# Kernel optimization log

Measured on AMD Instinct MI355X. Metric: run time of the kernel, lower is better.

Reference implementation:

```python
import jax, jax.numpy as jnp
import numpy as np
from math import sqrt

RATIOS = [0.5, 1.0, 2.0]
SCALES = [128.0, 256.0, 512.0]
STRIDE = 16
NA = 9  # len(RATIOS) * len(SCALES)


def _anchor_template():
    # matches RPNHead.__init__: center at stride/2, w = s/sqrt(r), h = s*sqrt(r)
    t = np.zeros((NA, 4), np.float32)
    for ri, r in enumerate(RATIOS):
        for si, s in enumerate(SCALES):
            i = ri * len(RATIOS) + si
            sr = sqrt(r)
            t[i] = [STRIDE / 2.0, STRIDE / 2.0, s / sr, s * sr]
    return jnp.asarray(t)


def _conv(x, w, b, pad):
    y = jax.lax.conv_general_dilated(
        x, w, window_strides=(1, 1), padding=[(pad, pad), (pad, pad)],
        dimension_numbers=('NCHW', 'OIHW', 'NCHW'))
    return y + b[None, :, None, None]


def setup_inputs() -> dict:
    key = jax.random.key(0)
    ks = jax.random.split(key, 5)
    B, C, H, W = 8, 512, 64, 64
    return {
        'feature_maps': jax.random.normal(ks[0], (B, C, H, W), jnp.float32),
        'img_size': jnp.ones((B, 2), jnp.int32) * 1024,  # (width, height) per image
        'conv_w': jax.random.normal(ks[1], (512, 512, 3, 3), jnp.float32) * 0.01,
        'conv_b': jnp.zeros((512,), jnp.float32),
        'cls_w': jax.random.normal(ks[2], (2 * NA, 512, 1, 1), jnp.float32) * 0.01,
        'cls_b': jnp.zeros((2 * NA,), jnp.float32),
        'reg_w': jax.random.normal(ks[3], (4 * NA, 512, 1, 1), jnp.float32) * 0.01,
        'reg_b': jnp.zeros((4 * NA,), jnp.float32),
    }


def reference(feature_maps, img_size, conv_w, conv_b, cls_w, cls_b, reg_w, reg_b):
    f = jax.nn.relu(_conv(feature_maps, conv_w, conv_b, 1))  # [B,512,H,W]
    B, _, H, W = f.shape
    # heads, NCHW -> NHWC, split anchor dim
    cls = _conv(f, cls_w, cls_b, 0).transpose(0, 2, 3, 1).reshape(B, H, W, NA, 2)
    reg = _conv(f, reg_w, reg_b, 0).transpose(0, 2, 3, 1).reshape(B, H, W, NA, 4)

    # generate_anchors (eval mode: anchors_ignore stays zero)
    tmpl = _anchor_template()  # [NA,4] xywh
    gy, gx = jnp.meshgrid(jnp.arange(H), jnp.arange(W), indexing='ij')
    center = jnp.stack([gx, gy], axis=-1).astype(jnp.float32) * STRIDE  # [H,W,2] (x,y)
    axy = tmpl[None, None, :, :2] + center[:, :, None, :]               # [H,W,NA,2]
    awh = jnp.broadcast_to(tmpl[None, None, :, 2:], (H, W, NA, 2))
    anchors = jnp.concatenate([axy, awh], axis=-1).reshape(-1, 4)       # [A,4]

    A = anchors.shape[0]
    reg = reg.reshape(B, A, 4)
    cls_scores = cls.reshape(B, A, 2)

    # anchor2bbox: inverse of the delta encoding in loss()
    ax, ay, aw, ah = anchors[:, 0], anchors[:, 1], anchors[:, 2], anchors[:, 3]
    px = ax[None, :] + reg[..., 0] * aw[None, :]
    py = ay[None, :] + reg[..., 1] * ah[None, :]
    pw = aw[None, :] * jnp.exp(reg[..., 2])
    ph = ah[None, :] * jnp.exp(reg[..., 3])
    imw = img_size[:, 0:1].astype(jnp.float32)
    imh = img_size[:, 1:2].astype(jnp.float32)
    x1 = jnp.clip(px - pw / 2, 0.0, imw)
    y1 = jnp.clip(py - ph / 2, 0.0, imh)
    x2 = jnp.clip(px + pw / 2, 0.0, imw)
    y2 = jnp.clip(py + ph / 2, 0.0, imh)
    proposals = jnp.stack([x1, y1, x2, y2], axis=-1)  # [B,A,4]

    anchors_ignore = jnp.zeros((B, A), jnp.int32)
    return (proposals, cls_scores, anchors_ignore)
```

## Files before the change

kernel.cpp:

```cpp
#include <hip/hip_runtime.h>
#include <hip/hip_bf16.h>
#include <stdint.h>

typedef __attribute__((ext_vector_type(4))) float f32x4;
typedef __attribute__((ext_vector_type(8))) short short8;

#define NB 8
#define NC 512
#define HP 66
#define WP 66
#define NPOS 32768
#define KTOT 4608
#define NKT 72

#define XP_ELEMS (NB*HP*WP*NC)
#define WR_ELEMS (NC*KTOT)
#define WC2_ELEMS (64*NC)
#define PROP_OFF 0
#define CLS_OFF  1179648
#define A_PER_B  36864

__device__ __forceinline__ short bf16bits(float v) {
    __hip_bfloat16 b = __float2bfloat16(v);
    return *reinterpret_cast<short*>(&b);
}
__device__ __forceinline__ void gload16(const short* g, short* l) {
    __builtin_amdgcn_global_load_lds(
        (const __attribute__((address_space(1))) unsigned int*)g,
        (__attribute__((address_space(3))) unsigned int*)l, 16, 0, 0);
}
#define BARRIER() asm volatile("s_barrier" ::: "memory")
#define VMCNT4()  asm volatile("s_waitcnt vmcnt(4)" ::: "memory")
#define VMCNT0()  asm volatile("s_waitcnt vmcnt(0)" ::: "memory")

__global__ void prep_input(const float* __restrict__ x, short* __restrict__ Xp) {
    __shared__ float t[64][65];
    const int pb = blockIdx.x, cb = blockIdx.y, b = blockIdx.z;
    const int tid = threadIdx.x;
    const int tx = tid & 63, ty = tid >> 6;
    const float* src = x + ((size_t)(b*NC + cb*64))*4096 + pb*64;
#pragma unroll
    for (int r = 0; r < 16; ++r) {
        int ch = ty + r*4;
        t[ch][tx] = src[(size_t)ch*4096 + tx];
    }
    __syncthreads();
#pragma unroll
    for (int rr = 0; rr < 2; ++rr) {
        int item = tid + rr*256;
        int pl = item >> 3, ck = item & 7;
        short8 v;
#pragma unroll
        for (int e = 0; e < 8; ++e) v[e] = bf16bits(t[ck*8+e][pl]);
        *(short8*)&Xp[((size_t)((b*HP + pb + 1)*WP) + (pl + 1))*NC + cb*64 + ck*8] = v;
    }
}

__global__ void prep_w(const float* __restrict__ w, short* __restrict__ Wr) {
    __shared__ float t[4608];
    const int o = blockIdx.x;
    const int tid = threadIdx.x;
    const float* src = w + (size_t)o*4608;
    for (int i = tid; i < 4608; i += 256) t[i] = src[i];
    __syncthreads();
#pragma unroll
    for (int k = 0; k < 9; ++k) {
#pragma unroll
        for (int c = 0; c < 2; ++c) {
            int ci = tid + c*256;
            Wr[(size_t)o*4608 + k*512 + ci] = bf16bits(t[ci*9 + k]);
        }
    }
}

__global__ void prep_w2(const float* __restrict__ cls_w, const float* __restrict__ reg_w,
                        short* __restrict__ Wc2) {
    int tid = blockIdx.x*256 + threadIdx.x;
    int row = tid >> 9, ci = tid & 511;
    float v = 0.f;
    if (row < 18)      v = cls_w[row*NC + ci];
    else if (row < 54) v = reg_w[(row-18)*NC + ci];
    Wc2[tid] = bf16bits(v);
}

__launch_bounds__(512, 2)
__global__ void conv3x3_gemm(const short* __restrict__ Xp, const short* __restrict__ Wr,
                             const float* __restrict__ bias, short* __restrict__ f) {
    extern __shared__ short lds[];
    const int tid = threadIdx.x;
    const int lane = tid & 63, wv = tid >> 6;
    const int bid = blockIdx.x;
    const int wg = (bid & 7) * 32 + (bid >> 3);
    const int pbase  = (wg >> 1) * 256;
    const int cobase = (wg & 1) * 256;
    const int wm = wv >> 2, wn = wv & 3;

    const int g_data = (tid & 7) ^ ((tid >> 3) & 7);
    int abase[4], bbase[4];
#pragma unroll
    for (int q = 0; q < 4; ++q) {
        int p = pbase + q*64 + (tid >> 3);
        int b = p >> 12, h = (p >> 6) & 63, w = p & 63;
        abase[q] = ((b*HP + h)*WP + w)*NC + g_data*8;
        bbase[q] = (cobase + q*64 + (tid >> 3))*KTOT + g_data*8;
    }
    const int stoff = tid*8;

    const int l15 = lane & 15, l4 = lane >> 4, l7 = lane & 7;
    const int kidx0 = (l4 ^ l7) * 8;
    const int kidx1 = ((4 + l4) ^ l7) * 8;
    const int Aroff = wm*8192 + l15*64;
    const int Broff = 16384 + (wn>>1)*8192 + (wn&1)*4096 + l15*64;

    auto stageA = [&](int t, int hh) {
        int seg = t >> 3;
        int dh = seg / 3, dw = seg - dh*3;
        int off = (dh*WP + dw)*NC + (t & 7)*64;
        short* dst = lds + (t & 1)*32768 + hh*8192 + stoff;
        gload16(Xp + abase[hh*2+0] + off, dst);
        gload16(Xp + abase[hh*2+1] + off, dst + 4096);
    };
    auto stageB = [&](int t, int hh) {
        int off = t * 64;
        short* dst = lds + (t & 1)*32768 + 16384 + hh*8192 + stoff;
        gload16(Wr + bbase[hh*2+0] + off, dst);
        gload16(Wr + bbase[hh*2+1] + off, dst + 4096);
    };

    f32x4 acc[8][4];
#pragma unroll
    for (int i = 0; i < 8; ++i)
#pragma unroll
        for (int j = 0; j < 4; ++j) acc[i][j] = (f32x4){0.f,0.f,0.f,0.f};

    short8 af[2][2], bfr[4][2];
    auto readA = [&](int bufb, int i2) {
        const short* Ab = lds + bufb*32768 + Aroff;
#pragma unroll
        for (int ii = 0; ii < 2; ++ii) {
            af[ii][0] = *(const short8*)(Ab + (i2+ii)*1024 + kidx0);
            af[ii][1] = *(const short8*)(Ab + (i2+ii)*1024 + kidx1);
        }
    };
    auto readB = [&](int bufb) {
        const short* Bb = lds + bufb*32768 + Broff;
#pragma unroll
        for (int j = 0; j < 4; ++j) {
            bfr[j][0] = *(const short8*)(Bb + j*1024 + kidx0);
            bfr[j][1] = *(const short8*)(Bb + j*1024 + kidx1);
        }
    };
    auto mfmaQ = [&](int i2) {
        __builtin_amdgcn_s_setprio(1);
#pragma unroll
        for (int kk = 0; kk < 2; ++kk)
#pragma unroll
            for (int ii = 0; ii < 2; ++ii)
#pragma unroll
                for (int j = 0; j < 4; ++j)
                    acc[i2+ii][j] = __builtin_amdgcn_mfma_f32_16x16x32_bf16(
                        af[ii][kk], bfr[j][kk], acc[i2+ii][j], 0, 0, 0);
        __builtin_amdgcn_s_setprio(0);
    };

    stageB(0,0); stageB(0,1); stageA(0,0); stageA(0,1); stageB(1,0); stageB(1,1);
    VMCNT4(); BARRIER();

    for (int it = 0; it < 36; ++it) {
        const int t1 = 2*it+1, t2 = 2*it+2, t3 = 2*it+3;
        const bool s2 = (t2 < NKT), s3 = (t3 < NKT);
        readB(0); readA(0, 0);
        stageA(t1, 0);
        BARRIER(); mfmaQ(0); BARRIER();
        readA(0, 2);
        stageA(t1, 1);
        BARRIER(); mfmaQ(2); BARRIER();
        readA(0, 4);
        if (s2) stageB(t2, 0);
        BARRIER(); mfmaQ(4); BARRIER();
        readA(0, 6);
        if (s2) stageB(t2, 1);
        BARRIER(); mfmaQ(6);
        if (s2) { VMCNT4(); } else { VMCNT0(); }
        BARRIER();
        readB(1); readA(1, 0);
        if (s2) stageA(t2, 0);
        BARRIER(); mfmaQ(0); BARRIER();
        readA(1, 2);
        if (s2) stageA(t2, 1);
        BARRIER(); mfmaQ(2); BARRIER();
        readA(1, 4);
        if (s3) stageB(t3, 0);
        BARRIER(); mfmaQ(4); BARRIER();
        readA(1, 6);
        if (s3) stageB(t3, 1);
        BARRIER(); mfmaQ(6);
        if (s3) { VMCNT4(); } else { VMCNT0(); }
        BARRIER();
    }

#pragma unroll
    for (int j = 0; j < 4; ++j) {
        const int col = cobase + wn*64 + j*16 + l15;
        const float bb = bias[col];
#pragma unroll
        for (int i = 0; i < 8; ++i) {
#pragma unroll
            for (int r = 0; r < 4; ++r) {
                int row = pbase + wm*128 + i*16 + l4*4 + r;
                float v = acc[i][j][r] + bb;
                v = v > 0.f ? v : 0.f;
                f[(size_t)row*NC + col] = bf16bits(v);
            }
        }
    }
}

__device__ const float AW_T[9] = {
    181.01933598375618f, 362.03867196751236f, 724.0773439350247f,
    128.f, 256.f, 512.f,
    90.50966799187809f, 181.01933598375618f, 362.03867196751236f };
__device__ const float AH_T[9] = {
    90.50966799187809f, 181.01933598375618f, 362.03867196751236f,
    128.f, 256.f, 512.f,
    181.01933598375618f, 362.03867196751236f, 724.0773439350247f };

__launch_bounds__(256)
__global__ void head_decode(const short* __restrict__ f, const short* __restrict__ Wc2,
                            const float* __restrict__ cls_b, const float* __restrict__ reg_b,
                            const int* __restrict__ img, float* __restrict__ out) {
    __shared__ float sm[64*65];
    const int tid = threadIdx.x, lane = tid & 63, wv = tid >> 6;
    const int p0 = blockIdx.x * 64;
    const int prow = lane & 15;
    const int kgrp = (lane >> 4) * 8;

    f32x4 acc[4];
#pragma unroll
    for (int j = 0; j < 4; ++j) acc[j] = (f32x4){0.f, 0.f, 0.f, 0.f};

    const short* arow = f + (size_t)(p0 + wv*16 + prow)*NC + kgrp;
#pragma unroll
    for (int k0 = 0; k0 < NC; k0 += 32) {
        short8 a = *(const short8*)(arow + k0);
#pragma unroll
        for (int j = 0; j < 4; ++j) {
            short8 b = *(const short8*)(Wc2 + (size_t)(j*16 + prow)*NC + k0 + kgrp);
            acc[j] = __builtin_amdgcn_mfma_f32_16x16x32_bf16(a, b, acc[j], 0, 0, 0);
        }
    }
    const int crow0 = wv*16 + (lane >> 4)*4;
#pragma unroll
    for (int j = 0; j < 4; ++j)
#pragma unroll
        for (int r = 0; r < 4; ++r)
            sm[(crow0 + r)*65 + j*16 + (lane & 15)] = acc[j][r];
    __syncthreads();

    for (int item = tid; item < 64*9; item += 256) {
        int pl = item / 9, a = item - pl*9;
        int p = p0 + pl;
        int b = p >> 12, h = (p >> 6) & 63, w = p & 63;
        float c0 = sm[pl*65 + a*2 + 0] + cls_b[a*2 + 0];
        float c1 = sm[pl*65 + a*2 + 1] + cls_b[a*2 + 1];
        float r0 = sm[pl*65 + 18 + a*4 + 0] + reg_b[a*4 + 0];
        float r1 = sm[pl*65 + 18 + a*4 + 1] + reg_b[a*4 + 1];
        float r2 = sm[pl*65 + 18 + a*4 + 2] + reg_b[a*4 + 2];
        float r3 = sm[pl*65 + 18 + a*4 + 3] + reg_b[a*4 + 3];
        float aw = AW_T[a], ah = AH_T[a];
        float ax = 8.f + 16.f*w, ay = 8.f + 16.f*h;
        float px = ax + r0*aw,  py = ay + r1*ah;
        float pw = aw*__expf(r2), ph = ah*__expf(r3);
        float imw = (float)img[b*2 + 0], imh = (float)img[b*2 + 1];
        float x1 = fminf(fmaxf(px - 0.5f*pw, 0.f), imw);
        float y1 = fminf(fmaxf(py - 0.5f*ph, 0.f), imh);
        float x2 = fminf(fmaxf(px + 0.5f*pw, 0.f), imw);
        float y2 = fminf(fmaxf(py + 0.5f*ph, 0.f), imh);
        int ag = (h*64 + w)*9 + a;
        float4* prop = (float4*)(out + PROP_OFF + ((size_t)b*A_PER_B + ag)*4);
        *prop = make_float4(x1, y1, x2, y2);
        float2* cs = (float2*)(out + CLS_OFF + ((size_t)b*A_PER_B + ag)*2);
        *cs = make_float2(c0, c1);
    }
}

extern "C" void kernel_launch(void* const* d_in, const int* in_sizes, int n_in,
                              void* d_out, int out_size, void* d_ws, size_t ws_size,
                              hipStream_t stream) {
    const float* x      = (const float*)d_in[0];
    const int*   img    = (const int*)  d_in[1];
    const float* conv_w = (const float*)d_in[2];
    const float* conv_b = (const float*)d_in[3];
    const float* cls_w  = (const float*)d_in[4];
    const float* cls_b  = (const float*)d_in[5];
    const float* reg_w  = (const float*)d_in[6];
    const float* reg_b  = (const float*)d_in[7];
    float* out = (float*)d_out;

    short* Xp  = (short*)d_ws;
    short* Wr  = Xp  + XP_ELEMS;
    short* Wc2 = Wr  + WR_ELEMS;
    short* f   = Wc2 + WC2_ELEMS;

    hipMemsetAsync(Xp, 0, (size_t)XP_ELEMS*2, stream);
    hipMemsetAsync(d_out, 0, (size_t)out_size*4, stream);

    prep_input<<<dim3(64,8,8), 256, 0, stream>>>(x, Xp);
    prep_w <<<512, 256, 0, stream>>>(conv_w, Wr);
    prep_w2<<<128, 256, 0, stream>>>(cls_w, reg_w, Wc2);

    hipFuncSetAttribute((const void*)conv3x3_gemm,
                        hipFuncAttributeMaxDynamicSharedMemorySize, 131072);
    conv3x3_gemm<<<256, 512, 131072, stream>>>(Xp, Wr, conv_b, f);
    head_decode <<<NPOS/64, 256, 0, stream>>>(f, Wc2, cls_b, reg_b, img, out);
}
```

Baseline: 283.0 us.

## Fuse 3x3 conv GEMM with 1x1 heads and decode, retile to full channel width

Each 3x3 conv workgroup now covers 128 positions across all 512 output channels. The ReLU'd bf16 feature tile stays in swizzled LDS, and the cls/reg 1x1 heads plus the box decode run in the same kernel, so the intermediate feature map is never written to and read back from global memory. The K loop now uses 32-wide steps with a double-buffered A tile and a triple-buffered B tile. The full memsets are replaced by a small kernel that zeroes only the padding border and the anchors_ignore region, and the head-weight packing moves into that kernel too. In exchange, every workgroup re-reads the 512x4608 weight matrix with a taller tile and runs 144 smaller K steps with more barriers.

Measured after the change: 265.9 us. 6.0% less time.

```diff
diff --git a/kernel.cpp b/kernel.cpp
--- a/kernel.cpp
+++ b/kernel.cpp
@@ -11,13 +11,14 @@
 #define WP 66
 #define NPOS 32768
 #define KTOT 4608
-#define NKT 72
+#define NT 144
 
 #define XP_ELEMS (NB*HP*WP*NC)
 #define WR_ELEMS (NC*KTOT)
 #define WC2_ELEMS (64*NC)
 #define PROP_OFF 0
 #define CLS_OFF  1179648
+#define ANCH_OFF 1769472
 #define A_PER_B  36864
 
 __device__ __forceinline__ short bf16bits(float v) {
@@ -73,146 +74,32 @@
     }
 }
 
-__global__ void prep_w2(const float* __restrict__ cls_w, const float* __restrict__ reg_w,
-                        short* __restrict__ Wc2) {
-    int tid = blockIdx.x*256 + threadIdx.x;
-    int row = tid >> 9, ci = tid & 511;
-    float v = 0.f;
-    if (row < 18)      v = cls_w[row*NC + ci];
-    else if (row < 54) v = reg_w[(row-18)*NC + ci];
-    Wc2[tid] = bf16bits(v);
-}
-
-__launch_bounds__(512, 2)
-__global__ void conv3x3_gemm(const short* __restrict__ Xp, const short* __restrict__ Wr,
-                             const float* __restrict__ bias, short* __restrict__ f) {
-    extern __shared__ short lds[];
-    const int tid = threadIdx.x;
-    const int lane = tid & 63, wv = tid >> 6;
-    const int bid = blockIdx.x;
-    const int wg = (bid & 7) * 32 + (bid >> 3);
-    const int pbase  = (wg >> 1) * 256;
-    const int cobase = (wg & 1) * 256;
-    const int wm = wv >> 2, wn = wv & 3;
-
-    const int g_data = (tid & 7) ^ ((tid >> 3) & 7);
-    int abase[4], bbase[4];
-#pragma unroll
-    for (int q = 0; q < 4; ++q) {
-        int p = pbase + q*64 + (tid >> 3);
-        int b = p >> 12, h = (p >> 6) & 63, w = p & 63;
-        abase[q] = ((b*HP + h)*WP + w)*NC + g_data*8;
-        bbase[q] = (cobase + q*64 + (tid >> 3))*KTOT + g_data*8;
-    }
-    const int stoff = tid*8;
-
-    const int l15 = lane & 15, l4 = lane >> 4, l7 = lane & 7;
-    const int kidx0 = (l4 ^ l7) * 8;
-    const int kidx1 = ((4 + l4) ^ l7) * 8;
-    const int Aroff = wm*8192 + l15*64;
-    const int Broff = 16384 + (wn>>1)*8192 + (wn&1)*4096 + l15*64;
-
-    auto stageA = [&](int t, int hh) {
-        int seg = t >> 3;
-        int dh = seg / 3, dw = seg - dh*3;
-        int off = (dh*WP + dw)*NC + (t & 7)*64;
-        short* dst = lds + (t & 1)*32768 + hh*8192 + stoff;
-        gload16(Xp + abase[hh*2+0] + off, dst);
-        gload16(Xp + abase[hh*2+1] + off, dst + 4096);
-    };
-    auto stageB = [&](int t, int hh) {
-        int off = t * 64;
-        short* dst = lds + (t & 1)*32768 + 16384 + hh*8192 + stoff;
-        gload16(Wr + bbase[hh*2+0] + off, dst);
-        gload16(Wr + bbase[hh*2+1] + off, dst + 4096);
-    };
-
-    f32x4 acc[8][4];
-#pragma unroll
-    for (int i = 0; i < 8; ++i)
-#pragma unroll
-        for (int j = 0; j < 4; ++j) acc[i][j] = (f32x4){0.f,0.f,0.f,0.f};
-
-    short8 af[2][2], bfr[4][2];
-    auto readA = [&](int bufb, int i2) {
-        const short* Ab = lds + bufb*32768 + Aroff;
-#pragma unroll
-        for (int ii = 0; ii < 2; ++ii) {
-            af[ii][0] = *(const short8*)(Ab + (i2+ii)*1024 + kidx0);
-            af[ii][1] = *(const short8*)(Ab + (i2+ii)*1024 + kidx1);
-        }
-    };
-    auto readB = [&](int bufb) {
-        const short* Bb = lds + bufb*32768 + Broff;
-#pragma unroll
-        for (int j = 0; j < 4; ++j) {
-            bfr[j][0] = *(const short8*)(Bb + j*1024 + kidx0);
-            bfr[j][1] = *(const short8*)(Bb + j*1024 + kidx1);
-        }
-    };
-    auto mfmaQ = [&](int i2) {
-        __builtin_amdgcn_s_setprio(1);
-#pragma unroll
-        for (int kk = 0; kk < 2; ++kk)
-#pragma unroll
-            for (int ii = 0; ii < 2; ++ii)
-#pragma unroll
-                for (int j = 0; j < 4; ++j)
-                    acc[i2+ii][j] = __builtin_amdgcn_mfma_f32_16x16x32_bf16(
-                        af[ii][kk], bfr[j][kk], acc[i2+ii][j], 0, 0, 0);
-        __builtin_amdgcn_s_setprio(0);
-    };
-
-    stageB(0,0); stageB(0,1); stageA(0,0); stageA(0,1); stageB(1,0); stageB(1,1);
-    VMCNT4(); BARRIER();
-
-    for (int it = 0; it < 36; ++it) {
-        const int t1 = 2*it+1, t2 = 2*it+2, t3 = 2*it+3;
-        const bool s2 = (t2 < NKT), s3 = (t3 < NKT);
-        readB(0); readA(0, 0);
-        stageA(t1, 0);
-        BARRIER(); mfmaQ(0); BARRIER();
-        readA(0, 2);
-        stageA(t1, 1);
-        BARRIER(); mfmaQ(2); BARRIER();
-        readA(0, 4);
-        if (s2) stageB(t2, 0);
-        BARRIER(); mfmaQ(4); BARRIER();
-        readA(0, 6);
-        if (s2) stageB(t2, 1);
-        BARRIER(); mfmaQ(6);
-        if (s2) { VMCNT4(); } else { VMCNT0(); }
-        BARRIER();
-        readB(1); readA(1, 0);
-        if (s2) stageA(t2, 0);
-        BARRIER(); mfmaQ(0); BARRIER();
-        readA(1, 2);
-        if (s2) stageA(t2, 1);
-        BARRIER(); mfmaQ(2); BARRIER();
-        readA(1, 4);
-        if (s3) stageB(t3, 0);
-        BARRIER(); mfmaQ(4); BARRIER();
-        readA(1, 6);
-        if (s3) stageB(t3, 1);
-        BARRIER(); mfmaQ(6);
-        if (s3) { VMCNT4(); } else { VMCNT0(); }
-        BARRIER();
-    }
-
-#pragma unroll
-    for (int j = 0; j < 4; ++j) {
-        const int col = cobase + wn*64 + j*16 + l15;
-        const float bb = bias[col];
-#pragma unroll
-        for (int i = 0; i < 8; ++i) {
-#pragma unroll
-            for (int r = 0; r < 4; ++r) {
-                int row = pbase + wm*128 + i*16 + l4*4 + r;
-                float v = acc[i][j][r] + bb;
-                v = v > 0.f ? v : 0.f;
-                f[(size_t)row*NC + col] = bf16bits(v);
-            }
-        }
+__global__ void prep_misc(const float* __restrict__ cls_w, const float* __restrict__ reg_w,
+                          short* __restrict__ Wc2, short* __restrict__ Xp,
+                          float* __restrict__ out) {
+    const int bid = blockIdx.x, tid = threadIdx.x;
+    if (bid < 128) {
+        int t = bid*256 + tid;
+        int row = t >> 9, ci = t & 511;
+        float v = 0.f;
+        if (row < 18)      v = cls_w[row*NC + ci];
+        else if (row < 54) v = reg_w[(row-18)*NC + ci];
+        Wc2[t] = bf16bits(v);
+    } else if (bid < 648) {
+        int idx = (bid-128)*256 + tid;
+        int b = idx / 16640;
+        int rem = idx - b*16640;
+        int r = rem >> 6, g = rem & 63;
+        int h, w;
+        if      (r < 66)  { h = 0;       w = r; }
+        else if (r < 132) { h = 65;      w = r - 66; }
+        else if (r < 196) { h = r - 131; w = 0; }
+        else              { h = r - 195; w = 65; }
+        short8 z = (short8){0,0,0,0,0,0,0,0};
+        *(short8*)&Xp[((size_t)((b*HP + h)*WP) + w)*NC + g*8] = z;
+    } else {
+        int idx = (bid-648)*256 + tid;
+        ((float4*)(out + ANCH_OFF))[idx] = make_float4(0.f,0.f,0.f,0.f);
     }
 }
 
@@ -225,41 +112,168 @@
     128.f, 256.f, 512.f,
     181.01933598375618f, 362.03867196751236f, 724.0773439350247f };
 
-__launch_bounds__(256)
-__global__ void head_decode(const short* __restrict__ f, const short* __restrict__ Wc2,
-                            const float* __restrict__ cls_b, const float* __restrict__ reg_b,
-                            const int* __restrict__ img, float* __restrict__ out) {
-    __shared__ float sm[64*65];
-    const int tid = threadIdx.x, lane = tid & 63, wv = tid >> 6;
-    const int p0 = blockIdx.x * 64;
-    const int prow = lane & 15;
-    const int kgrp = (lane >> 4) * 8;
-
-    f32x4 acc[4];
-#pragma unroll
-    for (int j = 0; j < 4; ++j) acc[j] = (f32x4){0.f, 0.f, 0.f, 0.f};
-
-    const short* arow = f + (size_t)(p0 + wv*16 + prow)*NC + kgrp;
-#pragma unroll
-    for (int k0 = 0; k0 < NC; k0 += 32) {
-        short8 a = *(const short8*)(arow + k0);
+__launch_bounds__(512, 2)
+__global__ void conv_fused(const short* __restrict__ Xp, const short* __restrict__ Wr,
+                           const float* __restrict__ bias, const short* __restrict__ Wc2,
+                           const float* __restrict__ cls_b, const float* __restrict__ reg_b,
+                           const int* __restrict__ img, float* __restrict__ out) {
+    extern __shared__ short lds[];
+    short* Ab0 = lds;            short* Ab1 = lds + 4096;
+    short* Bb0 = lds + 8192;     short* Bb1 = lds + 8192 + 16384;
+    short* Bb2 = lds + 8192 + 32768;
+    short* ABUF[2] = {Ab0, Ab1};
+    short* BBUF[3] = {Bb0, Bb1, Bb2};
+
+    const int tid = threadIdx.x;
+    const int lane = tid & 63, wv = tid >> 6;
+    const int bid = blockIdx.x;
+    const int wg = (bid & 7) * 32 + (bid >> 3);
+    const int pbase = wg * 128;
+    const int wm = wv >> 2, wn = wv & 3;
+    const int l15 = lane & 15, lg = lane >> 4;
+
+    const int G = ((tid & 3) - (tid >> 3)) & 3;
+    int aoff;
+    {
+        int p = pbase + (tid >> 2);
+        int b = p >> 12, h = (p >> 6) & 63, w = p & 63;
+        aoff = ((b*HP + h)*WP + w)*NC + G*8;
+    }
+    const int boff = (tid >> 2)*KTOT + G*8;
+    const int sdst = tid*8;
+
+    const int sigma = (((lg + ((l15 >> 1) & 3)) & 3)) * 8;
+
+    f32x4 acc[4][8];
+#pragma unroll
+    for (int i = 0; i < 4; ++i)
+#pragma unroll
+        for (int j = 0; j < 8; ++j) acc[i][j] = (f32x4){0.f,0.f,0.f,0.f};
+
+    short8 af_[4], bf_[8];
+
+    auto stageA = [&](int t, short* dst) {
+        int seg = t >> 4;
+        int dh = seg/3, dw = seg - dh*3;
+        gload16(Xp + aoff + (dh*WP + dw)*NC + (t & 15)*32, dst + sdst);
+    };
+    auto stageB2 = [&](int t, short* dst, int q0) {
+#pragma unroll
+        for (int q = q0; q < q0+2; ++q)
+            gload16(Wr + boff + q*128*KTOT + t*32, dst + q*4096 + sdst);
+    };
+    auto phA = [&](short* Ar, short* Br, bool sA, short* Aw, bool sB, short* Bw, int t) {
+#pragma unroll
+        for (int j = 0; j < 8; ++j)
+            bf_[j] = *(const short8*)(Br + (wn*128 + j*16 + l15)*32 + sigma);
+#pragma unroll
+        for (int ii = 0; ii < 2; ++ii)
+            af_[ii] = *(const short8*)(Ar + (wm*64 + ii*16 + l15)*32 + sigma);
+        if (sA) stageA(t+1, Aw);
+        if (sB) stageB2(t+2, Bw, 0);
+        BARRIER();
+        __builtin_amdgcn_s_setprio(1);
+#pragma unroll
+        for (int ii = 0; ii < 2; ++ii)
+#pragma unroll
+            for (int j = 0; j < 8; ++j)
+                acc[ii][j] = __builtin_amdgcn_mfma_f32_16x16x32_bf16(
+                    af_[ii], bf_[j], acc[ii][j], 0, 0, 0);
+        __builtin_amdgcn_s_setprio(0);
+        BARRIER();
+    };
+    auto phB = [&](short* Ar, bool sB, short* Bw, int t, int vm) {
+#pragma unroll
+        for (int ii = 2; ii < 4; ++ii)
+            af_[ii] = *(const short8*)(Ar + (wm*64 + ii*16 + l15)*32 + sigma);
+        if (sB) stageB2(t+2, Bw, 2);
+        BARRIER();
+        __builtin_amdgcn_s_setprio(1);
+#pragma unroll
+        for (int ii = 2; ii < 4; ++ii)
+#pragma unroll
+            for (int j = 0; j < 8; ++j)
+                acc[ii][j] = __builtin_amdgcn_mfma_f32_16x16x32_bf16(
+                    af_[ii], bf_[j], acc[ii][j], 0, 0, 0);
+        __builtin_amdgcn_s_setprio(0);
+        if (vm == 4) { VMCNT4(); } else if (vm == 0) { VMCNT0(); }
+        BARRIER();
+    };
+
+    stageB2(0, Bb0, 0); stageB2(0, Bb0, 2);
+    stageA(0, Ab0);
+    stageB2(1, Bb1, 0); stageB2(1, Bb1, 2);
+    VMCNT4(); BARRIER();
+
+#pragma unroll 1
+    for (int itt = 0; itt < 23; ++itt) {
+        const int t0 = itt*6;
+#pragma unroll
+        for (int c = 0; c < 6; ++c) {
+            const int t = t0 + c;
+            phA(ABUF[c&1], BBUF[c%3], true, ABUF[(c+1)&1], true, BBUF[(c+2)%3], t);
+            phB(ABUF[c&1], true, BBUF[(c+2)%3], t, 4);
+        }
+    }
+    {
+#pragma unroll
+        for (int c = 0; c < 6; ++c) {
+            const int t = 138 + c;
+            const bool sA = (c < 5), sB = (c < 4);
+            const int vm = (c < 4) ? 4 : (c == 4 ? 0 : -1);
+            phA(ABUF[c&1], BBUF[c%3], sA, ABUF[(c+1)&1], sB, BBUF[(c+2)%3], t);
+            phB(ABUF[c&1], sB, BBUF[(c+2)%3], t, vm);
+        }
+    }
+
+#pragma unroll
+    for (int j = 0; j < 8; ++j) {
+        const int co = wn*128 + j*16 + l15;
+        const float bb = bias[co];
+        const int g64 = co >> 3, e = co & 7;
+#pragma unroll
+        for (int i = 0; i < 4; ++i) {
+#pragma unroll
+            for (int r = 0; r < 4; ++r) {
+                const int prow = wm*64 + i*16 + lg*4 + r;
+                float v = acc[i][j][r] + bb;
+                v = v > 0.f ? v : 0.f;
+                const int slot = (g64 & 56) | ((g64 ^ prow) & 7);
+                lds[prow*512 + slot*8 + e] = bf16bits(v);
+            }
+        }
+    }
+    __syncthreads();
+
+    f32x4 acc2[4];
+#pragma unroll
+    for (int j = 0; j < 4; ++j) acc2[j] = (f32x4){0.f,0.f,0.f,0.f};
+    const int hrow = wv*16 + l15;
+#pragma unroll
+    for (int k0 = 0; k0 < 16; ++k0) {
+        const int g64 = k0*4 + lg;
+        const int slot = (g64 & 56) | ((g64 ^ hrow) & 7);
+        short8 a2 = *(const short8*)&lds[hrow*512 + slot*8];
 #pragma unroll
         for (int j = 0; j < 4; ++j) {
-            short8 b = *(const short8*)(Wc2 + (size_t)(j*16 + prow)*NC + k0 + kgrp);
-            acc[j] = __builtin_amdgcn_mfma_f32_16x16x32_bf16(a, b, acc[j], 0, 0, 0);
-        }
-    }
-    const int crow0 = wv*16 + (lane >> 4)*4;
+            short8 b2 = *(const short8*)&Wc2[(size_t)(j*16 + l15)*NC + k0*32 + lg*8];
+            acc2[j] = __builtin_amdgcn_mfma_f32_16x16x32_bf16(a2, b2, acc2[j], 0, 0, 0);
+        }
+    }
+    __syncthreads();
+
+    float* sm = (float*)lds;
+    const int crow0 = wv*16 + lg*4;
 #pragma unroll
     for (int j = 0; j < 4; ++j)
 #pragma unroll
         for (int r = 0; r < 4; ++r)
-            sm[(crow0 + r)*65 + j*16 + (lane & 15)] = acc[j][r];
-    __syncthreads();
-
-    for (int item = tid; item < 64*9; item += 256) {
+            sm[(crow0 + r)*65 + j*16 + l15] = acc2[j][r];
+    __syncthreads();
+
+    for (int item = tid; item < 1152; item += 512) {
         int pl = item / 9, a = item - pl*9;
-        int p = p0 + pl;
+        int p = pbase + pl;
         int b = p >> 12, h = (p >> 6) & 63, w = p & 63;
         float c0 = sm[pl*65 + a*2 + 0] + cls_b[a*2 + 0];
         float c1 = sm[pl*65 + a*2 + 1] + cls_b[a*2 + 1];
@@ -300,17 +314,13 @@
     short* Xp  = (short*)d_ws;
     short* Wr  = Xp  + XP_ELEMS;
     short* Wc2 = Wr  + WR_ELEMS;
-    short* f   = Wc2 + WC2_ELEMS;
-
-    hipMemsetAsync(Xp, 0, (size_t)XP_ELEMS*2, stream);
-    hipMemsetAsync(d_out, 0, (size_t)out_size*4, stream);
-
+
+    prep_misc<<<936, 256, 0, stream>>>(cls_w, reg_w, Wc2, Xp, out);
     prep_input<<<dim3(64,8,8), 256, 0, stream>>>(x, Xp);
     prep_w <<<512, 256, 0, stream>>>(conv_w, Wr);
-    prep_w2<<<128, 256, 0, stream>>>(cls_w, reg_w, Wc2);
-
-    hipFuncSetAttribute((const void*)conv3x3_gemm,
+
+    hipFuncSetAttribute((const void*)conv_fused,
                         hipFuncAttributeMaxDynamicSharedMemorySize, 131072);
-    conv3x3_gemm<<<256, 512, 131072, stream>>>(Xp, Wr, conv_b, f);
-    head_decode <<<NPOS/64, 256, 0, stream>>>(f, Wc2, cls_b, reg_b, img, out);
-}
+    conv_fused<<<256, 512, 131072, stream>>>(Xp, Wr, conv_b, Wc2,
+                                             cls_b, reg_b, img, out);
+}
```

## Fuse 1x1 head GEMM into conv epilogue and merge prep kernels

Applied to the files above, without the earlier changes.

The 1x1 cls/reg head GEMM now runs inside the conv kernel's epilogue. Each block stages its ReLU'd bf16 tile in LDS, multiplies it by its half of the head weights, and writes fp32 partial sums per channel half. A light combine kernel adds the two halves and decodes the boxes. This removes the full bf16 feature-map round trip to global memory. The three prep kernels are also merged into one launch that zeroes only the padding border, replacing the full Xp memset and the output memset. The trade-offs are a larger fp32 partial buffer and extra epilogue work in the conv kernel.

After: 248.1 us. -12.3%, faster.

```diff
diff --git a/kernel.cpp b/kernel.cpp
--- a/kernel.cpp
+++ b/kernel.cpp
@@ -18,6 +18,7 @@
 #define WC2_ELEMS (64*NC)
 #define PROP_OFF 0
 #define CLS_OFF  1179648
+#define ANCH_OFF 1769472
 #define A_PER_B  36864
 
 __device__ __forceinline__ short bf16bits(float v) {
@@ -33,59 +34,73 @@
 #define VMCNT4()  asm volatile("s_waitcnt vmcnt(4)" ::: "memory")
 #define VMCNT0()  asm volatile("s_waitcnt vmcnt(0)" ::: "memory")
 
-__global__ void prep_input(const float* __restrict__ x, short* __restrict__ Xp) {
-    __shared__ float t[64][65];
-    const int pb = blockIdx.x, cb = blockIdx.y, b = blockIdx.z;
-    const int tid = threadIdx.x;
-    const int tx = tid & 63, ty = tid >> 6;
-    const float* src = x + ((size_t)(b*NC + cb*64))*4096 + pb*64;
-#pragma unroll
-    for (int r = 0; r < 16; ++r) {
-        int ch = ty + r*4;
-        t[ch][tx] = src[(size_t)ch*4096 + tx];
-    }
-    __syncthreads();
-#pragma unroll
-    for (int rr = 0; rr < 2; ++rr) {
-        int item = tid + rr*256;
-        int pl = item >> 3, ck = item & 7;
-        short8 v;
-#pragma unroll
-        for (int e = 0; e < 8; ++e) v[e] = bf16bits(t[ck*8+e][pl]);
-        *(short8*)&Xp[((size_t)((b*HP + pb + 1)*WP) + (pl + 1))*NC + cb*64 + ck*8] = v;
-    }
-}
-
-__global__ void prep_w(const float* __restrict__ w, short* __restrict__ Wr) {
-    __shared__ float t[4608];
-    const int o = blockIdx.x;
-    const int tid = threadIdx.x;
-    const float* src = w + (size_t)o*4608;
-    for (int i = tid; i < 4608; i += 256) t[i] = src[i];
-    __syncthreads();
-#pragma unroll
-    for (int k = 0; k < 9; ++k) {
-#pragma unroll
-        for (int c = 0; c < 2; ++c) {
-            int ci = tid + c*256;
-            Wr[(size_t)o*4608 + k*512 + ci] = bf16bits(t[ci*9 + k]);
-        }
-    }
-}
-
-__global__ void prep_w2(const float* __restrict__ cls_w, const float* __restrict__ reg_w,
-                        short* __restrict__ Wc2) {
-    int tid = blockIdx.x*256 + threadIdx.x;
-    int row = tid >> 9, ci = tid & 511;
-    float v = 0.f;
-    if (row < 18)      v = cls_w[row*NC + ci];
-    else if (row < 54) v = reg_w[(row-18)*NC + ci];
-    Wc2[tid] = bf16bits(v);
+__global__ void prep_all(const float* __restrict__ x, const float* __restrict__ conv_w,
+                         const float* __restrict__ cls_w, const float* __restrict__ reg_w,
+                         short* __restrict__ Wr, short* __restrict__ Wc2,
+                         short* __restrict__ Xp) {
+    __shared__ float smem[4608];
+    const int bid = blockIdx.x, tid = threadIdx.x;
+    if (bid < 4096) {
+        float (*t)[65] = (float(*)[65])smem;
+        const int pb = bid & 63, cb = (bid >> 6) & 7, b = bid >> 9;
+        const int tx = tid & 63, ty = tid >> 6;
+        const float* src = x + ((size_t)(b*NC + cb*64))*4096 + pb*64;
+#pragma unroll
+        for (int r = 0; r < 16; ++r) {
+            int ch = ty + r*4;
+            t[ch][tx] = src[(size_t)ch*4096 + tx];
+        }
+        __syncthreads();
+#pragma unroll
+        for (int rr = 0; rr < 2; ++rr) {
+            int item = tid + rr*256;
+            int pl = item >> 3, ck = item & 7;
+            short8 v;
+#pragma unroll
+            for (int e = 0; e < 8; ++e) v[e] = bf16bits(t[ck*8+e][pl]);
+            *(short8*)&Xp[((size_t)((b*HP + pb + 1)*WP) + (pl + 1))*NC + cb*64 + ck*8] = v;
+        }
+    } else if (bid < 4608) {
+        const int o = bid - 4096;
+        const float* src = conv_w + (size_t)o*4608;
+        for (int i = tid; i < 4608; i += 256) smem[i] = src[i];
+        __syncthreads();
+#pragma unroll
+        for (int k = 0; k < 9; ++k)
+#pragma unroll
+            for (int c = 0; c < 2; ++c) {
+                int ci = tid + c*256;
+                Wr[(size_t)o*4608 + k*512 + ci] = bf16bits(smem[ci*9 + k]);
+            }
+    } else {
+        const int m = bid - 4608;
+        if (m < 128) {
+            int t = m*256 + tid;
+            int row = t >> 9, ci = t & 511;
+            float v = 0.f;
+            if (row < 18)      v = cls_w[row*NC + ci];
+            else if (row < 54) v = reg_w[(row-18)*NC + ci];
+            Wc2[t] = bf16bits(v);
+        } else {
+            int idx = (m-128)*256 + tid;
+            int b = idx / 16640;
+            int rem = idx - b*16640;
+            int r = rem >> 6, g = rem & 63;
+            int h, w;
+            if      (r < 66)  { h = 0;       w = r; }
+            else if (r < 132) { h = 65;      w = r - 66; }
+            else if (r < 196) { h = r - 131; w = 0; }
+            else              { h = r - 195; w = 65; }
+            short8 z = (short8){0,0,0,0,0,0,0,0};
+            *(short8*)&Xp[((size_t)((b*HP + h)*WP) + w)*NC + g*8] = z;
+        }
+    }
 }
 
 __launch_bounds__(512, 2)
-__global__ void conv3x3_gemm(const short* __restrict__ Xp, const short* __restrict__ Wr,
-                             const float* __restrict__ bias, short* __restrict__ f) {
+__global__ void conv_fused(const short* __restrict__ Xp, const short* __restrict__ Wr,
+                           const float* __restrict__ bias, const short* __restrict__ Wc2,
+                           float* __restrict__ partial) {
     extern __shared__ short lds[];
     const int tid = threadIdx.x;
     const int lane = tid & 63, wv = tid >> 6;
@@ -198,22 +213,61 @@
         if (s3) { VMCNT4(); } else { VMCNT0(); }
         BARRIER();
     }
+    __syncthreads();
 
 #pragma unroll
     for (int j = 0; j < 4; ++j) {
-        const int col = cobase + wn*64 + j*16 + l15;
-        const float bb = bias[col];
+        const int ch = wn*64 + j*16 + l15;
+        const float bb = bias[cobase + ch];
+        const int g = ch >> 3, e = ch & 7;
 #pragma unroll
         for (int i = 0; i < 8; ++i) {
 #pragma unroll
             for (int r = 0; r < 4; ++r) {
-                int row = pbase + wm*128 + i*16 + l4*4 + r;
+                const int pos = wm*128 + i*16 + l4*4 + r;
                 float v = acc[i][j][r] + bb;
                 v = v > 0.f ? v : 0.f;
-                f[(size_t)row*NC + col] = bf16bits(v);
+                const int slot = (g & 24) | ((g ^ pos) & 7);
+                lds[pos*256 + slot*8 + e] = bf16bits(v);
             }
         }
     }
+    __syncthreads();
+
+    f32x4 acc2[2][4];
+#pragma unroll
+    for (int i2 = 0; i2 < 2; ++i2)
+#pragma unroll
+        for (int j2 = 0; j2 < 4; ++j2) acc2[i2][j2] = (f32x4){0.f,0.f,0.f,0.f};
+    const int hbase = wv*32;
+#pragma unroll
+    for (int kk = 0; kk < 8; ++kk) {
+        short8 b2[4];
+#pragma unroll
+        for (int j2 = 0; j2 < 4; ++j2)
+            b2[j2] = *(const short8*)&Wc2[(size_t)(j2*16 + l15)*NC + cobase + kk*32 + l4*8];
+#pragma unroll
+        for (int i2 = 0; i2 < 2; ++i2) {
+            const int pos = hbase + i2*16 + l15;
+            const int g = kk*4 + l4;
+            const int slot = (g & 24) | ((g ^ pos) & 7);
+            short8 a2 = *(const short8*)&lds[pos*256 + slot*8];
+#pragma unroll
+            for (int j2 = 0; j2 < 4; ++j2)
+                acc2[i2][j2] = __builtin_amdgcn_mfma_f32_16x16x32_bf16(
+                    a2, b2[j2], acc2[i2][j2], 0, 0, 0);
+        }
+    }
+
+    const int half = wg & 1;
+    float* pdst = partial + ((size_t)half*NPOS + pbase + hbase)*64;
+#pragma unroll
+    for (int i2 = 0; i2 < 2; ++i2)
+#pragma unroll
+        for (int j2 = 0; j2 < 4; ++j2)
+#pragma unroll
+            for (int r = 0; r < 4; ++r)
+                pdst[(i2*16 + l4*4 + r)*64 + j2*16 + l15] = acc2[i2][j2][r];
 }
 
 __device__ const float AW_T[9] = {
@@ -226,38 +280,27 @@
     181.01933598375618f, 362.03867196751236f, 724.0773439350247f };
 
 __launch_bounds__(256)
-__global__ void head_decode(const short* __restrict__ f, const short* __restrict__ Wc2,
-                            const float* __restrict__ cls_b, const float* __restrict__ reg_b,
-                            const int* __restrict__ img, float* __restrict__ out) {
+__global__ void combine_decode(const float* __restrict__ partial,
+                               const float* __restrict__ cls_b, const float* __restrict__ reg_b,
+                               const int* __restrict__ img, float* __restrict__ out) {
     __shared__ float sm[64*65];
-    const int tid = threadIdx.x, lane = tid & 63, wv = tid >> 6;
+    const int tid = threadIdx.x;
     const int p0 = blockIdx.x * 64;
-    const int prow = lane & 15;
-    const int kgrp = (lane >> 4) * 8;
-
-    f32x4 acc[4];
-#pragma unroll
-    for (int j = 0; j < 4; ++j) acc[j] = (f32x4){0.f, 0.f, 0.f, 0.f};
-
-    const short* arow = f + (size_t)(p0 + wv*16 + prow)*NC + kgrp;
-#pragma unroll
-    for (int k0 = 0; k0 < NC; k0 += 32) {
-        short8 a = *(const short8*)(arow + k0);
-#pragma unroll
-        for (int j = 0; j < 4; ++j) {
-            short8 b = *(const short8*)(Wc2 + (size_t)(j*16 + prow)*NC + k0 + kgrp);
-            acc[j] = __builtin_amdgcn_mfma_f32_16x16x32_bf16(a, b, acc[j], 0, 0, 0);
-        }
-    }
-    const int crow0 = wv*16 + (lane >> 4)*4;
-#pragma unroll
-    for (int j = 0; j < 4; ++j)
-#pragma unroll
-        for (int r = 0; r < 4; ++r)
-            sm[(crow0 + r)*65 + j*16 + (lane & 15)] = acc[j][r];
+    const float4* pa = (const float4*)partial;
+#pragma unroll
+    for (int q = 0; q < 4; ++q) {
+        int idx = tid + q*256;
+        int pl = idx >> 4, n4 = idx & 15;
+        float4 a = pa[(size_t)(p0 + pl)*16 + n4];
+        float4 b = pa[(size_t)(NPOS + p0 + pl)*16 + n4];
+        sm[pl*65 + n4*4 + 0] = a.x + b.x;
+        sm[pl*65 + n4*4 + 1] = a.y + b.y;
+        sm[pl*65 + n4*4 + 2] = a.z + b.z;
+        sm[pl*65 + n4*4 + 3] = a.w + b.w;
+    }
     __syncthreads();
 
-    for (int item = tid; item < 64*9; item += 256) {
+    for (int item = tid; item < 576; item += 256) {
         int pl = item / 9, a = item - pl*9;
         int p = p0 + pl;
         int b = p >> 12, h = (p >> 6) & 63, w = p & 63;
@@ -281,6 +324,7 @@
         *prop = make_float4(x1, y1, x2, y2);
         float2* cs = (float2*)(out + CLS_OFF + ((size_t)b*A_PER_B + ag)*2);
         *cs = make_float2(c0, c1);
+        out[ANCH_OFF + (size_t)b*A_PER_B + ag] = 0.0f;
     }
 }
 
@@ -297,20 +341,15 @@
     const float* reg_b  = (const float*)d_in[7];
     float* out = (float*)d_out;
 
-    short* Xp  = (short*)d_ws;
-    short* Wr  = Xp  + XP_ELEMS;
-    short* Wc2 = Wr  + WR_ELEMS;
-    short* f   = Wc2 + WC2_ELEMS;
-
-    hipMemsetAsync(Xp, 0, (size_t)XP_ELEMS*2, stream);
-    hipMemsetAsync(d_out, 0, (size_t)out_size*4, stream);
-
-    prep_input<<<dim3(64,8,8), 256, 0, stream>>>(x, Xp);
-    prep_w <<<512, 256, 0, stream>>>(conv_w, Wr);
-    prep_w2<<<128, 256, 0, stream>>>(cls_w, reg_w, Wc2);
-
-    hipFuncSetAttribute((const void*)conv3x3_gemm,
+    short* Xp      = (short*)d_ws;
+    short* Wr      = Xp  + XP_ELEMS;
+    short* Wc2     = Wr  + WR_ELEMS;
+    float* partial = (float*)(Wc2 + WC2_ELEMS);
+
+    prep_all<<<5256, 256, 0, stream>>>(x, conv_w, cls_w, reg_w, Wr, Wc2, Xp);
+
+    hipFuncSetAttribute((const void*)conv_fused,
                         hipFuncAttributeMaxDynamicSharedMemorySize, 131072);
-    conv3x3_gemm<<<256, 512, 131072, stream>>>(Xp, Wr, conv_b, f);
-    head_decode <<<NPOS/64, 256, 0, stream>>>(f, Wc2, cls_b, reg_b, img, out);
-}
+    conv_fused<<<256, 512, 131072, stream>>>(Xp, Wr, conv_b, Wc2, partial);
+    combine_decode<<<NPOS/64, 256, 0, stream>>>(partial, cls_b, reg_b, img, out);
+}
```
